# Kernel tuning notes

Measured on AMD Instinct MI355X. Metric: run time of the kernel, lower is better.

## Reference

```python
import jax, jax.numpy as jnp
import numpy as np

E = 1408      # hidden_size
H = 16        # num heads
D = E // H    # head_dim = 88
S = 1025      # (448/14)^2 + 1 cls token
B = 8


def setup_inputs() -> dict:
    key = jax.random.key(0)
    ks = jax.random.split(key, 11)
    scale = 1.0 / np.sqrt(E)
    inp = {
        "hidden_states": jax.random.normal(ks[0], (B, S, E), dtype=jnp.float32),
    }
    # rotary freqs as cos/sin of random angles, shape (S, D//2)
    theta = jax.random.uniform(ks[1], (S, D // 2), dtype=jnp.float32) * (2.0 * np.pi)
    inp["freqs_cos"] = jnp.cos(theta)
    inp["freqs_sin"] = jnp.sin(theta)
    # projection weights stored torch-style: (out_features, in_features)
    inp["q_w"] = jax.random.normal(ks[2], (E, E), dtype=jnp.float32) * scale
    inp["q_b"] = jax.random.normal(ks[3], (E,), dtype=jnp.float32) * scale
    inp["k_w"] = jax.random.normal(ks[4], (E, E), dtype=jnp.float32) * scale
    inp["k_b"] = jax.random.normal(ks[5], (E,), dtype=jnp.float32) * scale
    inp["v_w"] = jax.random.normal(ks[6], (E, E), dtype=jnp.float32) * scale
    inp["v_b"] = jax.random.normal(ks[7], (E,), dtype=jnp.float32) * scale
    inp["o_w"] = jax.random.normal(ks[8], (E, E), dtype=jnp.float32) * scale
    inp["o_b"] = jax.random.normal(ks[9], (E,), dtype=jnp.float32) * scale
    return inp


def _apply_rope(x, cos, sin):
    # x: (B, S, H, D); interpret last dim as D//2 complex pairs (re, im)
    xr = x.astype(jnp.float32).reshape(*x.shape[:-1], D // 2, 2)
    re, im = xr[..., 0], xr[..., 1]
    c = cos[None, :, None, :]  # broadcast over batch and heads
    s = sin[None, :, None, :]
    out_re = re * c - im * s
    out_im = re * s + im * c
    return jnp.stack([out_re, out_im], axis=-1).reshape(x.shape).astype(x.dtype)


def reference(hidden_states, freqs_cos, freqs_sin, q_w, q_b, k_w, k_b, v_w, v_b, o_w, o_b):
    b, s, _ = hidden_states.shape
    q = (hidden_states @ q_w.T + q_b).reshape(b, s, H, D)
    k = (hidden_states @ k_w.T + k_b).reshape(b, s, H, D)
    v = (hidden_states @ v_w.T + v_b).reshape(b, s, H, D)
    q = _apply_rope(q, freqs_cos, freqs_sin)
    k = _apply_rope(k, freqs_cos, freqs_sin)
    # (B, H, S, D)
    q = q.transpose(0, 2, 1, 3)
    k = k.transpose(0, 2, 1, 3)
    v = v.transpose(0, 2, 1, 3)
    scores = jnp.einsum('bhqd,bhkd->bhqk', q, k) / np.sqrt(D)
    attn = jax.nn.softmax(scores.astype(jnp.float32), axis=-1).astype(q.dtype)
    out = jnp.einsum('bhqk,bhkd->bqhd', attn, v).reshape(b, s, H * D)
    out = out @ o_w.T + o_b
    return out, attn
```

## Files before the change

kernel.cpp:

```cpp
#include <hip/hip_runtime.h>

typedef unsigned short u16;
typedef __attribute__((ext_vector_type(8))) short short8;
typedef __attribute__((ext_vector_type(4))) float f32x4;
typedef __attribute__((ext_vector_type(16))) float f32x16;

#define E_DIM 1408
#define H_HEADS 16
#define S_SEQ 1025
#define B_BATCH 8
#define S_PAD 1088
#define D_PAD 128
#define M_ROWS 8200
#define M_PAD 8320

struct __attribute__((packed, aligned(4))) f4u { float x, y, z, w; };

__device__ __forceinline__ u16 f2bf(float f){
  union { float f; unsigned u; } x; x.f = f;
  unsigned r = x.u + 0x7fffu + ((x.u >> 16) & 1u);
  return (u16)(r >> 16);
}

__device__ __forceinline__ void gload16(const void* g, void* l){
  __builtin_amdgcn_global_load_lds(
      (const __attribute__((address_space(1))) void*)g,
      (__attribute__((address_space(3))) void*)l, 16, 0, 0);
}

__device__ __forceinline__ f32x4 mfma16(short8 a, short8 b, f32x4 c){
  return __builtin_amdgcn_mfma_f32_16x16x32_bf16(a, b, c, 0, 0, 0);
}
__device__ __forceinline__ f32x16 mfma32(short8 a, short8 b, f32x16 c){
  return __builtin_amdgcn_mfma_f32_32x32x16_bf16(a, b, c, 0, 0, 0);
}

__device__ __forceinline__ unsigned cvtpk(float a, float b){
  unsigned r;
  asm("v_cvt_pk_bf16_f32 %0, %1, %2" : "=v"(r) : "v"(a), "v"(b));
  return r;
}
__device__ __forceinline__ void plswap(unsigned &a, unsigned &b){
  asm("v_permlane32_swap_b32 %0, %1" : "+v"(a), "+v"(b));
}

__global__ __launch_bounds__(256) void cvt_kernel(const float* __restrict__ src,
                                                  u16* __restrict__ dst, int n8){
  int i = blockIdx.x * 256 + threadIdx.x;
  if (i >= n8) return;
  const float4* s4 = (const float4*)src;
  float4 a = s4[2*i], b = s4[2*i+1];
  union { u16 u[8]; short8 v; } o;
  o.u[0]=f2bf(a.x); o.u[1]=f2bf(a.y); o.u[2]=f2bf(a.z); o.u[3]=f2bf(a.w);
  o.u[4]=f2bf(b.x); o.u[5]=f2bf(b.y); o.u[6]=f2bf(b.z); o.u[7]=f2bf(b.w);
  ((short8*)dst)[i] = o.v;
}

__global__ __launch_bounds__(256) void cvt4_kernel(const float* __restrict__ s0,
                                                   const float* __restrict__ s1,
                                                   const float* __restrict__ s2,
                                                   const float* __restrict__ s3,
                                                   u16* __restrict__ dst, int n8){
  int i = blockIdx.x * 256 + threadIdx.x;
  if (i >= n8) return;
  const float* src = (blockIdx.y == 0) ? s0 : (blockIdx.y == 1) ? s1
                   : (blockIdx.y == 2) ? s2 : s3;
  u16* d = dst + (size_t)blockIdx.y * n8 * 8;
  const float4* s4 = (const float4*)src;
  float4 a = s4[2*i], b = s4[2*i+1];
  union { u16 u[8]; short8 v; } o;
  o.u[0]=f2bf(a.x); o.u[1]=f2bf(a.y); o.u[2]=f2bf(a.z); o.u[3]=f2bf(a.w);
  o.u[4]=f2bf(b.x); o.u[5]=f2bf(b.y); o.u[6]=f2bf(b.z); o.u[7]=f2bf(b.w);
  ((short8*)d)[i] = o.v;
}

__global__ __launch_bounds__(256) void zero_pads_kernel(u16* __restrict__ Q,
                                                        u16* __restrict__ K,
                                                        u16* __restrict__ Vt){
  int i = blockIdx.x * 256 + threadIdx.x;
  const int n1 = 128 * S_PAD * 8;
  const int n2 = 128 * 63 * 96;
  const int n3 = 128 * 96 * 63;
  if (i < n1){
    int d = 88 + (i & 7); int t = i >> 3;
    int s = t % S_PAD; int bh = t / S_PAD;
    size_t o = ((size_t)bh * S_PAD + s) * D_PAD + d;
    Q[o] = 0; K[o] = 0;
  } else if (i < n1 + n2){
    int j = i - n1;
    int d = j % 96; int t = j / 96;
    int s = 1025 + t % 63; int bh = t / 63;
    size_t o = ((size_t)bh * S_PAD + s) * D_PAD + d;
    Q[o] = 0; K[o] = 0;
  } else if (i < n1 + n2 + n3){
    int j = i - n1 - n2;
    int d = j % 96; int t = j / 96;
    int sp = 1025 + t % 63; int bh = t / 63;
    Vt[((size_t)bh * D_PAD + d) * S_PAD + sp] = 0;
  }
}

template<int MODE>
__global__ __launch_bounds__(256) void gemm_bt(
    const u16* __restrict__ A, const u16* __restrict__ W,
    const float* __restrict__ b_q, const float* __restrict__ b_k,
    const float* __restrict__ b_v,
    u16* __restrict__ Qb, u16* __restrict__ Kb, u16* __restrict__ Vtb,
    float* __restrict__ outF,
    const float* __restrict__ fcos, const float* __restrict__ fsin)
{
  __shared__ u16 As[128*32];
  __shared__ u16 Bs[128*32];
  const int tid = threadIdx.x;
  const int lane = tid & 63, wid = tid >> 6;
  const int cl = lane & 15, grp = lane >> 4;

  const int nwg = (int)(gridDim.x * gridDim.y);
  const int orig = blockIdx.x + gridDim.x * blockIdx.y;
  const int qq = nwg >> 3, rr = nwg & 7;
  const int xcd = orig & 7, kk = orig >> 3;
  const int wg = (xcd < rr ? xcd * (qq + 1) : rr * (qq + 1) + (xcd - rr) * qq) + kk;
  const int bx = wg % (int)gridDim.x, by = wg / (int)gridDim.x;

  const int n0 = bx * 128, m0 = by * 128;
  const int region = (MODE == 0) ? (bx / 11) : 0;
  const int wm = (wid >> 1) * 64, wn = (wid & 1) * 64;
  f32x4 acc[4][4] = {};

  for (int k0 = 0; k0 < E_DIM; k0 += 32){
    __syncthreads();
#pragma unroll
    for (int rd = 0; rd < 2; ++rd){
      int G = rd * 256 + tid;
      int row = G >> 2, cg = G & 3;
      gload16(A + (size_t)(m0 + row) * E_DIM + k0 + cg * 8, (char*)As + (size_t)G * 16);
      gload16(W + (size_t)(n0 + row) * E_DIM + k0 + cg * 8, (char*)Bs + (size_t)G * 16);
    }
    __syncthreads();
    short8 av[4], bv[4];
#pragma unroll
    for (int i = 0; i < 4; ++i) av[i] = *(const short8*)&As[(wm + i*16 + cl)*32 + grp*8];
#pragma unroll
    for (int j = 0; j < 4; ++j) bv[j] = *(const short8*)&Bs[(wn + j*16 + cl)*32 + grp*8];
    __builtin_amdgcn_s_setprio(1);
#pragma unroll
    for (int i = 0; i < 4; ++i)
#pragma unroll
      for (int j = 0; j < 4; ++j)
        acc[i][j] = mfma16(av[i], bv[j], acc[i][j]);
    __builtin_amdgcn_s_setprio(0);
  }

  const float* bias = (MODE == 1) ? b_q : (region == 0 ? b_q : (region == 1 ? b_k : b_v));
  const float QSCALE = 0.15379181f;

#pragma unroll
  for (int i = 0; i < 4; ++i){
#pragma unroll
    for (int j = 0; j < 4; ++j){
      const int jcol = n0 + wn + j*16 + cl;
      const int jl = jcol - region * E_DIM;
      const float bsv = bias[jl];
      const int hh = jl / 88;
      const int dd = jl - hh * 88;
#pragma unroll
      for (int r = 0; r < 4; ++r){
        const int rrow = m0 + wm + i*16 + grp*4 + r;
        float v = acc[i][j][r] + bsv;
        if (MODE == 0 && region <= 1){
          float other = __shfl_xor(v, 1);
          int bb = rrow / 1025;
          int spos = rrow - bb * 1025;
          int pp = dd >> 1;
          float c = fcos[spos * 44 + pp];
          float s = fsin[spos * 44 + pp];
          float o = fmaf(v, c, (jl & 1) ? (other * s) : -(other * s));
          if (region == 0) o *= QSCALE;
          if (rrow < M_ROWS){
            size_t dst = (((size_t)(bb * 16 + hh)) * S_PAD + spos) * D_PAD + dd;
            (region ? Kb : Qb)[dst] = f2bf(o);
          }
        } else if (MODE == 0){
          if (rrow < M_ROWS){
            int bb = rrow / 1025;
            int spos = rrow - bb * 1025;
            size_t dst = (((size_t)(bb * 16 + hh)) * D_PAD + dd) * S_PAD + spos;
            Vtb[dst] = f2bf(v);
          }
        } else {
          if (rrow < M_ROWS) outF[(size_t)rrow * E_DIM + jcol] = v;
        }
      }
    }
  }
}

#define STAGE_K(buf, kt)                                                        \
  {                                                                             \
    _Pragma("unroll")                                                           \
    for (int rd = 0; rd < 4; ++rd){                                             \
      int G = rd * 256 + tid;                                                   \
      int row = G >> 4, c = G & 15;                                             \
      gload16(Kg + (size_t)((kt) * 64 + row) * 128 + ((c ^ (row & 15)) * 8),    \
              (char*)&Ks[buf][0] + (size_t)G * 16);                             \
    }                                                                           \
  }

#define STAGE_V(kt)                                                             \
  {                                                                             \
    _Pragma("unroll")                                                           \
    for (int rd = 0; rd < 3; ++rd){                                             \
      int G = rd * 256 + tid;                                                   \
      int row = G >> 3, c = G & 7;                                              \
      gload16(Vg + (size_t)row * S_PAD + (kt) * 64 + ((c ^ (row & 7)) * 8),     \
              (char*)Vs + (size_t)G * 16);                                      \
    }                                                                           \
  }

__global__ __launch_bounds__(256, 3) void attn_kernel(
    const u16* __restrict__ Qb, const u16* __restrict__ Kb,
    const u16* __restrict__ Vtb, float* __restrict__ attn,
    u16* __restrict__ AO)
{
  __shared__ u16 Ks[2][64 * 128];
  __shared__ u16 Vs[96 * 64];
  const int tid = threadIdx.x, wid = tid >> 6, lane = tid & 63;
  const int q5 = lane & 31, hi = lane >> 5;
  int lin = blockIdx.x + gridDim.x * blockIdx.y;
  lin = (lin & 7) * 144 + (lin >> 3);
  const int qt = lin % 9, bh = lin / 9;
  const int b = bh >> 4, h = bh & 15;
  const u16* __restrict__ Qg = Qb + (size_t)bh * S_PAD * 128;
  const u16* __restrict__ Kg = Kb + (size_t)bh * S_PAD * 128;
  const u16* __restrict__ Vg = Vtb + (size_t)bh * 128 * S_PAD;
  const int qrow = qt * 128 + wid * 32 + q5;
  const int qrowc = (qrow < S_PAD) ? qrow : (S_PAD - 1);

  short8 qf[6];
#pragma unroll
  for (int ds = 0; ds < 6; ++ds)
    qf[ds] = *(const short8*)&Qg[(size_t)qrowc * 128 + ds * 16 + hi * 8];

  float l0 = 0.f, l1 = 0.f, l2 = 0.f, l3 = 0.f;
  STAGE_K(0, 0);
  __syncthreads();
  for (int kt = 0; kt < 17; ++kt){
    const int cur = kt & 1;
    if (kt < 16) STAGE_K(cur ^ 1, kt + 1);
#pragma unroll
    for (int ks = 0; ks < 2; ++ks){
      f32x16 sc = {};
      const int krow = ks * 32 + q5;
      __builtin_amdgcn_s_setprio(1);
#pragma unroll
      for (int ds = 0; ds < 6; ++ds){
        int c = ds * 2 + hi;
        short8 kf = *(const short8*)&Ks[cur][krow * 128 + ((c ^ (krow & 15)) * 8)];
        sc = mfma32(kf, qf[ds], sc);
      }
      __builtin_amdgcn_s_setprio(0);
#pragma unroll
      for (int r = 0; r < 16; r += 4){
        l0 += __builtin_amdgcn_exp2f(sc[r]);
        l1 += __builtin_amdgcn_exp2f(sc[r+1]);
        l2 += __builtin_amdgcn_exp2f(sc[r+2]);
        l3 += __builtin_amdgcn_exp2f(sc[r+3]);
      }
    }
    __syncthreads();
  }
  float l = (l0 + l1) + (l2 + l3);
  l += __shfl_xor(l, 32);
  l -= 63.0f;
  const float lg2l = __builtin_amdgcn_logf(l);

  f32x16 oacc[3] = {};
  STAGE_K(0, 0);
  STAGE_V(0);
  __syncthreads();
  for (int kt = 0; kt < 17; ++kt){
    const int cur = kt & 1;
    if (kt < 16) STAGE_K(cur ^ 1, kt + 1);
    short8 pa0[2], pa1[2];
#pragma unroll
    for (int ks = 0; ks < 2; ++ks){
      f32x16 sc = {};
      const int krow = ks * 32 + q5;
      __builtin_amdgcn_s_setprio(1);
#pragma unroll
      for (int ds = 0; ds < 6; ++ds){
        int c = ds * 2 + hi;
        short8 kf = *(const short8*)&Ks[cur][krow * 128 + ((c ^ (krow & 15)) * 8)];
        sc = mfma32(kf, qf[ds], sc);
      }
      __builtin_amdgcn_s_setprio(0);
#pragma unroll
      for (int r = 0; r < 16; ++r) sc[r] = __builtin_amdgcn_exp2f(sc[r] - lg2l);

      if (qrow < 1025){
        if (kt < 16){
          float* arow = attn + ((size_t)bh * 1025 + qrow) * 1025 + kt * 64 + ks * 32 + 4 * hi;
#pragma unroll
          for (int g = 0; g < 4; ++g){
            f4u w4 = { sc[4*g], sc[4*g+1], sc[4*g+2], sc[4*g+3] };
            *(f4u*)(arow + 8 * g) = w4;
          }
        } else {
#pragma unroll
          for (int r = 0; r < 16; ++r){
            int kabs = 1024 + ks * 32 + (r & 3) + 8 * (r >> 2) + 4 * hi;
            if (kabs < 1025)
              attn[((size_t)bh * 1025 + qrow) * 1025 + kabs] = sc[r];
          }
        }
      }

      unsigned w0 = cvtpk(sc[0],  sc[1]),  w1 = cvtpk(sc[2],  sc[3]);
      unsigned w2 = cvtpk(sc[4],  sc[5]),  w3 = cvtpk(sc[6],  sc[7]);
      unsigned w4 = cvtpk(sc[8],  sc[9]),  w5 = cvtpk(sc[10], sc[11]);
      unsigned w6 = cvtpk(sc[12], sc[13]), w7 = cvtpk(sc[14], sc[15]);
      plswap(w0, w2); plswap(w1, w3); plswap(w4, w6); plswap(w5, w7);
      union U { unsigned u[4]; short8 s8; } A0, A1;
      A0.u[0] = w0; A0.u[1] = w1; A0.u[2] = w2; A0.u[3] = w3;
      A1.u[0] = w4; A1.u[1] = w5; A1.u[2] = w6; A1.u[3] = w7;
      pa0[ks] = A0.s8; pa1[ks] = A1.s8;
    }

    __syncthreads();
    __builtin_amdgcn_s_setprio(1);
#pragma unroll
    for (int ks = 0; ks < 2; ++ks){
#pragma unroll
      for (int dt = 0; dt < 3; ++dt){
        const int vrow = dt * 32 + q5;
        int c0 = ks * 4 + hi;
        short8 vf0 = *(const short8*)&Vs[vrow * 64 + ((c0 ^ (vrow & 7)) * 8)];
        oacc[dt] = mfma32(pa0[ks], vf0, oacc[dt]);
        int c1 = ks * 4 + 2 + hi;
        short8 vf1 = *(const short8*)&Vs[vrow * 64 + ((c1 ^ (vrow & 7)) * 8)];
        oacc[dt] = mfma32(pa1[ks], vf1, oacc[dt]);
      }
    }
    __builtin_amdgcn_s_setprio(0);
    __syncthreads();
    if (kt < 16) STAGE_V(kt + 1);
  }

  const int qb0 = qt * 128 + wid * 32;
#pragma unroll
  for (int dt = 0; dt < 3; ++dt){
    const int d = dt * 32 + q5;
    if (d < 88){
#pragma unroll
      for (int r = 0; r < 16; ++r){
        int qq2 = qb0 + (r & 3) + 8 * (r >> 2) + 4 * hi;
        if (qq2 < 1025)
          AO[((size_t)b * 1025 + qq2) * E_DIM + h * 88 + d] = f2bf(oacc[dt][r]);
      }
    }
  }
}

extern "C" void kernel_launch(void* const* d_in, const int* in_sizes, int n_in,
                              void* d_out, int out_size, void* d_ws, size_t ws_size,
                              hipStream_t stream)
{
  const float* hs   = (const float*)d_in[0];
  const float* fcos = (const float*)d_in[1];
  const float* fsin = (const float*)d_in[2];
  const float* q_w  = (const float*)d_in[3];
  const float* q_b  = (const float*)d_in[4];
  const float* k_w  = (const float*)d_in[5];
  const float* k_b  = (const float*)d_in[6];
  const float* v_w  = (const float*)d_in[7];
  const float* v_b  = (const float*)d_in[8];
  const float* o_w  = (const float*)d_in[9];
  const float* o_b  = (const float*)d_in[10];
  float* out0 = (float*)d_out;
  float* attn = out0 + (size_t)B_BATCH * S_SEQ * E_DIM;

  char* ws = (char*)d_ws;
  size_t off = 0;
  auto take = [&](size_t bytes){
    char* p = ws + off; off += (bytes + 255) & ~(size_t)255; return p;
  };
  u16* Xb  = (u16*)take((size_t)M_PAD * E_DIM * 2);
  u16* Wb  = (u16*)take((size_t)4 * E_DIM * E_DIM * 2);
  u16* Qb  = (u16*)take((size_t)128 * S_PAD * D_PAD * 2);
  u16* Kb  = (u16*)take((size_t)128 * S_PAD * D_PAD * 2);
  u16* Vtb = (u16*)take((size_t)128 * D_PAD * S_PAD * 2);
  u16* AO  = (u16*)take((size_t)M_PAD * E_DIM * 2);

  cvt_kernel<<<(1443200 + 255) / 256, 256, 0, stream>>>(hs, Xb, 1443200);
  cvt4_kernel<<<dim3(968, 4), 256, 0, stream>>>(q_w, k_w, v_w, o_w, Wb, 247808);
  zero_pads_kernel<<<10400, 256, 0, stream>>>(Qb, Kb, Vtb);

  gemm_bt<0><<<dim3(33, 65), 256, 0, stream>>>(Xb, Wb, q_b, k_b, v_b,
                                               Qb, Kb, Vtb, nullptr, fcos, fsin);

  attn_kernel<<<dim3(9, 128), 256, 0, stream>>>(Qb, Kb, Vtb, attn, AO);

  gemm_bt<1><<<dim3(11, 65), 256, 0, stream>>>(AO, Wb + 3 * (size_t)E_DIM * E_DIM,
                                               o_b, o_b, o_b,
                                               nullptr, nullptr, nullptr, out0, fcos, fsin);
}
```

Before: 547.9 us.

## Widen attention blocks to 512 threads with double-buffered K/V prefetch pipeline

Measured after the change: 561.3 us. 2.5% more time.

```diff
diff --git a/kernel.cpp b/kernel.cpp
--- a/kernel.cpp
+++ b/kernel.cpp
@@ -13,6 +13,7 @@
 #define D_PAD 128
 #define M_ROWS 8200
 #define M_PAD 8320
+#define N_QKV 4224
 
 struct __attribute__((packed, aligned(4))) f4u { float x, y, z, w; };
 
@@ -43,6 +44,9 @@
 __device__ __forceinline__ void plswap(unsigned &a, unsigned &b){
   asm("v_permlane32_swap_b32 %0, %1" : "+v"(a), "+v"(b));
 }
+
+#define BARX() { asm volatile("" ::: "memory"); __builtin_amdgcn_s_barrier(); asm volatile("" ::: "memory"); }
+#define WAITV(n) asm volatile("s_waitcnt vmcnt(" #n ")" ::: "memory")
 
 __global__ __launch_bounds__(256) void cvt_kernel(const float* __restrict__ src,
                                                   u16* __restrict__ dst, int n8){
@@ -56,15 +60,13 @@
   ((short8*)dst)[i] = o.v;
 }
 
-__global__ __launch_bounds__(256) void cvt4_kernel(const float* __restrict__ s0,
+__global__ __launch_bounds__(256) void cvt3_kernel(const float* __restrict__ s0,
                                                    const float* __restrict__ s1,
                                                    const float* __restrict__ s2,
-                                                   const float* __restrict__ s3,
                                                    u16* __restrict__ dst, int n8){
   int i = blockIdx.x * 256 + threadIdx.x;
   if (i >= n8) return;
-  const float* src = (blockIdx.y == 0) ? s0 : (blockIdx.y == 1) ? s1
-                   : (blockIdx.y == 2) ? s2 : s3;
+  const float* src = (blockIdx.y == 0) ? s0 : (blockIdx.y == 1) ? s1 : s2;
   u16* d = dst + (size_t)blockIdx.y * n8 * 8;
   const float4* s4 = (const float4*)src;
   float4 a = s4[2*i], b = s4[2*i+1];
@@ -198,42 +200,44 @@
 #define STAGE_K(buf, kt)                                                        \
   {                                                                             \
     _Pragma("unroll")                                                           \
-    for (int rd = 0; rd < 4; ++rd){                                             \
-      int G = rd * 256 + tid;                                                   \
+    for (int rd = 0; rd < 2; ++rd){                                             \
+      int G = rd * 512 + tid;                                                   \
       int row = G >> 4, c = G & 15;                                             \
       gload16(Kg + (size_t)((kt) * 64 + row) * 128 + ((c ^ (row & 15)) * 8),    \
-              (char*)&Ks[buf][0] + (size_t)G * 16);                             \
+              (char*)Ks + (size_t)(buf) * 16384 + (size_t)G * 16);              \
     }                                                                           \
   }
 
-#define STAGE_V(kt)                                                             \
+#define STAGE_V(buf, kt)                                                        \
   {                                                                             \
     _Pragma("unroll")                                                           \
-    for (int rd = 0; rd < 3; ++rd){                                             \
-      int G = rd * 256 + tid;                                                   \
+    for (int rd = 0; rd < 2; ++rd){                                             \
+      int G = rd * 512 + tid;                                                   \
       int row = G >> 3, c = G & 7;                                              \
       gload16(Vg + (size_t)row * S_PAD + (kt) * 64 + ((c ^ (row & 7)) * 8),     \
-              (char*)Vs + (size_t)G * 16);                                      \
+              (char*)Vs + (size_t)(buf) * 16384 + (size_t)G * 16);              \
     }                                                                           \
   }
 
-__global__ __launch_bounds__(256, 3) void attn_kernel(
+__global__ __launch_bounds__(512, 4) void attn_kernel(
     const u16* __restrict__ Qb, const u16* __restrict__ Kb,
     const u16* __restrict__ Vtb, float* __restrict__ attn,
     u16* __restrict__ AO)
 {
-  __shared__ u16 Ks[2][64 * 128];
-  __shared__ u16 Vs[96 * 64];
+  __shared__ u16 sm[32768];
+  u16* const Ks = sm;
+  u16* const Vs = sm + 16384;
   const int tid = threadIdx.x, wid = tid >> 6, lane = tid & 63;
   const int q5 = lane & 31, hi = lane >> 5;
   int lin = blockIdx.x + gridDim.x * blockIdx.y;
-  lin = (lin & 7) * 144 + (lin >> 3);
-  const int qt = lin % 9, bh = lin / 9;
+  lin = (lin & 7) * 80 + (lin >> 3);
+  const int qt = lin % 5, bh = lin / 5;
   const int b = bh >> 4, h = bh & 15;
   const u16* __restrict__ Qg = Qb + (size_t)bh * S_PAD * 128;
   const u16* __restrict__ Kg = Kb + (size_t)bh * S_PAD * 128;
   const u16* __restrict__ Vg = Vtb + (size_t)bh * 128 * S_PAD;
-  const int qrow = qt * 128 + wid * 32 + q5;
+  const int qb0 = qt * 256 + wid * 32;
+  const int qrow = qb0 + q5;
   const int qrowc = (qrow < S_PAD) ? qrow : (S_PAD - 1);
 
   short8 qf[6];
@@ -243,10 +247,11 @@
 
   float l0 = 0.f, l1 = 0.f, l2 = 0.f, l3 = 0.f;
   STAGE_K(0, 0);
-  __syncthreads();
+  STAGE_K(1, 1);
+  WAITV(2);
+  BARX();
   for (int kt = 0; kt < 17; ++kt){
     const int cur = kt & 1;
-    if (kt < 16) STAGE_K(cur ^ 1, kt + 1);
 #pragma unroll
     for (int ks = 0; ks < 2; ++ks){
       f32x16 sc = {};
@@ -255,7 +260,7 @@
 #pragma unroll
       for (int ds = 0; ds < 6; ++ds){
         int c = ds * 2 + hi;
-        short8 kf = *(const short8*)&Ks[cur][krow * 128 + ((c ^ (krow & 15)) * 8)];
+        short8 kf = *(const short8*)&Ks[(size_t)cur * 8192 + krow * 128 + ((c ^ (krow & 15)) * 8)];
         sc = mfma32(kf, qf[ds], sc);
       }
       __builtin_amdgcn_s_setprio(0);
@@ -267,20 +272,31 @@
         l3 += __builtin_amdgcn_exp2f(sc[r+3]);
       }
     }
-    __syncthreads();
-  }
+    if (kt == 16) break;
+    BARX();
+    if (kt <= 14){
+      STAGE_K(cur, kt + 2);
+      WAITV(2);
+    } else {
+      STAGE_V(0, 0);
+      STAGE_V(1, 1);
+      WAITV(4);
+    }
+    BARX();
+  }
+  BARX();
+  STAGE_K(0, 0);
+  STAGE_K(1, 1);
   float l = (l0 + l1) + (l2 + l3);
   l += __shfl_xor(l, 32);
   l -= 63.0f;
   const float lg2l = __builtin_amdgcn_logf(l);
+  WAITV(2);
+  BARX();
 
   f32x16 oacc[3] = {};
-  STAGE_K(0, 0);
-  STAGE_V(0);
-  __syncthreads();
   for (int kt = 0; kt < 17; ++kt){
     const int cur = kt & 1;
-    if (kt < 16) STAGE_K(cur ^ 1, kt + 1);
     short8 pa0[2], pa1[2];
 #pragma unroll
     for (int ks = 0; ks < 2; ++ks){
@@ -290,7 +306,7 @@
 #pragma unroll
       for (int ds = 0; ds < 6; ++ds){
         int c = ds * 2 + hi;
-        short8 kf = *(const short8*)&Ks[cur][krow * 128 + ((c ^ (krow & 15)) * 8)];
+        short8 kf = *(const short8*)&Ks[(size_t)cur * 8192 + krow * 128 + ((c ^ (krow & 15)) * 8)];
         sc = mfma32(kf, qf[ds], sc);
       }
       __builtin_amdgcn_s_setprio(0);
@@ -326,7 +342,6 @@
       pa0[ks] = A0.s8; pa1[ks] = A1.s8;
     }
 
-    __syncthreads();
     __builtin_amdgcn_s_setprio(1);
 #pragma unroll
     for (int ks = 0; ks < 2; ++ks){
@@ -334,19 +349,27 @@
       for (int dt = 0; dt < 3; ++dt){
         const int vrow = dt * 32 + q5;
         int c0 = ks * 4 + hi;
-        short8 vf0 = *(const short8*)&Vs[vrow * 64 + ((c0 ^ (vrow & 7)) * 8)];
+        short8 vf0 = *(const short8*)&Vs[(size_t)cur * 8192 + vrow * 64 + ((c0 ^ (vrow & 7)) * 8)];
         oacc[dt] = mfma32(pa0[ks], vf0, oacc[dt]);
         int c1 = ks * 4 + 2 + hi;
-        short8 vf1 = *(const short8*)&Vs[vrow * 64 + ((c1 ^ (vrow & 7)) * 8)];
+        short8 vf1 = *(const short8*)&Vs[(size_t)cur * 8192 + vrow * 64 + ((c1 ^ (vrow & 7)) * 8)];
         oacc[dt] = mfma32(pa1[ks], vf1, oacc[dt]);
       }
     }
     __builtin_amdgcn_s_setprio(0);
-    __syncthreads();
-    if (kt < 16) STAGE_V(kt + 1);
-  }
-
-  const int qb0 = qt * 128 + wid * 32;
+
+    if (kt == 16) break;
+    BARX();
+    if (kt <= 14){
+      STAGE_K(cur, kt + 2);
+      STAGE_V(cur, kt + 2);
+      WAITV(4);
+    } else {
+      WAITV(0);
+    }
+    BARX();
+  }
+
 #pragma unroll
   for (int dt = 0; dt < 3; ++dt){
     const int d = dt * 32 + q5;
@@ -384,23 +407,24 @@
   auto take = [&](size_t bytes){
     char* p = ws + off; off += (bytes + 255) & ~(size_t)255; return p;
   };
-  u16* Xb  = (u16*)take((size_t)M_PAD * E_DIM * 2);
-  u16* Wb  = (u16*)take((size_t)4 * E_DIM * E_DIM * 2);
-  u16* Qb  = (u16*)take((size_t)128 * S_PAD * D_PAD * 2);
-  u16* Kb  = (u16*)take((size_t)128 * S_PAD * D_PAD * 2);
-  u16* Vtb = (u16*)take((size_t)128 * D_PAD * S_PAD * 2);
-  u16* AO  = (u16*)take((size_t)M_PAD * E_DIM * 2);
+  u16* Xb   = (u16*)take((size_t)M_PAD * E_DIM * 2);
+  u16* Wqkv = (u16*)take((size_t)N_QKV * E_DIM * 2);
+  u16* Wo   = (u16*)take((size_t)E_DIM * E_DIM * 2);
+  u16* Qb   = (u16*)take((size_t)128 * S_PAD * D_PAD * 2);
+  u16* Kb   = (u16*)take((size_t)128 * S_PAD * D_PAD * 2);
+  u16* Vtb  = (u16*)take((size_t)128 * D_PAD * S_PAD * 2);
+  u16* AO   = (u16*)take((size_t)M_PAD * E_DIM * 2);
 
   cvt_kernel<<<(1443200 + 255) / 256, 256, 0, stream>>>(hs, Xb, 1443200);
-  cvt4_kernel<<<dim3(968, 4), 256, 0, stream>>>(q_w, k_w, v_w, o_w, Wb, 247808);
+  cvt3_kernel<<<dim3(968, 3), 256, 0, stream>>>(q_w, k_w, v_w, Wqkv, 247808);
+  cvt_kernel<<<968, 256, 0, stream>>>(o_w, Wo, 247808);
   zero_pads_kernel<<<10400, 256, 0, stream>>>(Qb, Kb, Vtb);
 
-  gemm_bt<0><<<dim3(33, 65), 256, 0, stream>>>(Xb, Wb, q_b, k_b, v_b,
+  gemm_bt<0><<<dim3(33, 65), 256, 0, stream>>>(Xb, Wqkv, q_b, k_b, v_b,
                                                Qb, Kb, Vtb, nullptr, fcos, fsin);
 
-  attn_kernel<<<dim3(9, 128), 256, 0, stream>>>(Qb, Kb, Vtb, attn, AO);
-
-  gemm_bt<1><<<dim3(11, 65), 256, 0, stream>>>(AO, Wb + 3 * (size_t)E_DIM * E_DIM,
-                                               o_b, o_b, o_b,
+  attn_kernel<<<dim3(5, 128), 512, 0, stream>>>(Qb, Kb, Vtb, attn, AO);
+
+  gemm_bt<1><<<dim3(11, 65), 256, 0, stream>>>(AO, Wo, o_b, o_b, o_b,
                                                nullptr, nullptr, nullptr, out0, fcos, fsin);
 }
```

## Split V projection into transposed GEMM and pipeline attention loads with vmcnt waits

Applied to the files above, without the earlier changes.

Result: no change. 557.2 us (+1.7%).

```diff
diff --git a/kernel.cpp b/kernel.cpp
--- a/kernel.cpp
+++ b/kernel.cpp
@@ -13,6 +13,7 @@
 #define D_PAD 128
 #define M_ROWS 8200
 #define M_PAD 8320
+#define N_QKV 4224
 
 struct __attribute__((packed, aligned(4))) f4u { float x, y, z, w; };
 
@@ -43,6 +44,9 @@
 __device__ __forceinline__ void plswap(unsigned &a, unsigned &b){
   asm("v_permlane32_swap_b32 %0, %1" : "+v"(a), "+v"(b));
 }
+
+#define BARX() { asm volatile("" ::: "memory"); __builtin_amdgcn_s_barrier(); asm volatile("" ::: "memory"); }
+#define WAITV(n) asm volatile("s_waitcnt vmcnt(" #n ")" ::: "memory")
 
 __global__ __launch_bounds__(256) void cvt_kernel(const float* __restrict__ src,
                                                   u16* __restrict__ dst, int n8){
@@ -56,15 +60,13 @@
   ((short8*)dst)[i] = o.v;
 }
 
-__global__ __launch_bounds__(256) void cvt4_kernel(const float* __restrict__ s0,
+__global__ __launch_bounds__(256) void cvt3_kernel(const float* __restrict__ s0,
                                                    const float* __restrict__ s1,
                                                    const float* __restrict__ s2,
-                                                   const float* __restrict__ s3,
                                                    u16* __restrict__ dst, int n8){
   int i = blockIdx.x * 256 + threadIdx.x;
   if (i >= n8) return;
-  const float* src = (blockIdx.y == 0) ? s0 : (blockIdx.y == 1) ? s1
-                   : (blockIdx.y == 2) ? s2 : s3;
+  const float* src = (blockIdx.y == 0) ? s0 : (blockIdx.y == 1) ? s1 : s2;
   u16* d = dst + (size_t)blockIdx.y * n8 * 8;
   const float4* s4 = (const float4*)src;
   float4 a = s4[2*i], b = s4[2*i+1];
@@ -151,8 +153,32 @@
     __builtin_amdgcn_s_setprio(0);
   }
 
-  const float* bias = (MODE == 1) ? b_q : (region == 0 ? b_q : (region == 1 ? b_k : b_v));
   const float QSCALE = 0.15379181f;
+
+  if (MODE == 2){
+#pragma unroll
+    for (int j = 0; j < 4; ++j){
+      const int scol = n0 + wn + j*16 + cl;
+      const int bb = scol / 1025;
+      const int spos = scol - bb * 1025;
+      const bool ok = (scol < M_ROWS);
+#pragma unroll
+      for (int i = 0; i < 4; ++i){
+#pragma unroll
+        for (int r = 0; r < 4; ++r){
+          const int jl = m0 + wm + i*16 + grp*4 + r;
+          const int hh = jl / 88;
+          const int dd = jl - hh * 88;
+          float v = acc[i][j][r] + b_v[jl];
+          if (ok)
+            Vtb[(((size_t)(bb * 16 + hh)) * D_PAD + dd) * S_PAD + spos] = f2bf(v);
+        }
+      }
+    }
+    return;
+  }
+
+  const float* bias = (MODE == 1) ? b_q : (region == 0 ? b_q : b_k);
 
 #pragma unroll
   for (int i = 0; i < 4; ++i){
@@ -167,7 +193,7 @@
       for (int r = 0; r < 4; ++r){
         const int rrow = m0 + wm + i*16 + grp*4 + r;
         float v = acc[i][j][r] + bsv;
-        if (MODE == 0 && region <= 1){
+        if (MODE == 0){
           float other = __shfl_xor(v, 1);
           int bb = rrow / 1025;
           int spos = rrow - bb * 1025;
@@ -180,13 +206,6 @@
             size_t dst = (((size_t)(bb * 16 + hh)) * S_PAD + spos) * D_PAD + dd;
             (region ? Kb : Qb)[dst] = f2bf(o);
           }
-        } else if (MODE == 0){
-          if (rrow < M_ROWS){
-            int bb = rrow / 1025;
-            int spos = rrow - bb * 1025;
-            size_t dst = (((size_t)(bb * 16 + hh)) * D_PAD + dd) * S_PAD + spos;
-            Vtb[dst] = f2bf(v);
-          }
         } else {
           if (rrow < M_ROWS) outF[(size_t)rrow * E_DIM + jcol] = v;
         }
@@ -220,7 +239,7 @@
 __global__ __launch_bounds__(256, 3) void attn_kernel(
     const u16* __restrict__ Qb, const u16* __restrict__ Kb,
     const u16* __restrict__ Vtb, float* __restrict__ attn,
-    u16* __restrict__ AO)
+    u16* __restrict__ AO, float* __restrict__ dumpf)
 {
   __shared__ u16 Ks[2][64 * 128];
   __shared__ u16 Vs[96 * 64];
@@ -233,7 +252,8 @@
   const u16* __restrict__ Qg = Qb + (size_t)bh * S_PAD * 128;
   const u16* __restrict__ Kg = Kb + (size_t)bh * S_PAD * 128;
   const u16* __restrict__ Vg = Vtb + (size_t)bh * 128 * S_PAD;
-  const int qrow = qt * 128 + wid * 32 + q5;
+  const int qb0 = qt * 128 + wid * 32;
+  const int qrow = qb0 + q5;
   const int qrowc = (qrow < S_PAD) ? qrow : (S_PAD - 1);
 
   short8 qf[6];
@@ -243,10 +263,15 @@
 
   float l0 = 0.f, l1 = 0.f, l2 = 0.f, l3 = 0.f;
   STAGE_K(0, 0);
-  __syncthreads();
   for (int kt = 0; kt < 17; ++kt){
     const int cur = kt & 1;
-    if (kt < 16) STAGE_K(cur ^ 1, kt + 1);
+    if (kt < 16){
+      STAGE_K(cur ^ 1, kt + 1);
+      WAITV(4);
+    } else {
+      WAITV(0);
+    }
+    BARX();
 #pragma unroll
     for (int ks = 0; ks < 2; ++ks){
       f32x16 sc = {};
@@ -267,7 +292,7 @@
         l3 += __builtin_amdgcn_exp2f(sc[r+3]);
       }
     }
-    __syncthreads();
+    BARX();
   }
   float l = (l0 + l1) + (l2 + l3);
   l += __shfl_xor(l, 32);
@@ -277,10 +302,13 @@
   f32x16 oacc[3] = {};
   STAGE_K(0, 0);
   STAGE_V(0);
-  __syncthreads();
   for (int kt = 0; kt < 17; ++kt){
     const int cur = kt & 1;
     if (kt < 16) STAGE_K(cur ^ 1, kt + 1);
+    if (kt == 0)      { WAITV(7); }
+    else if (kt < 16) { WAITV(15); }
+    else              { WAITV(11); }
+    BARX();
     short8 pa0[2], pa1[2];
 #pragma unroll
     for (int ks = 0; ks < 2; ++ks){
@@ -297,21 +325,23 @@
 #pragma unroll
       for (int r = 0; r < 16; ++r) sc[r] = __builtin_amdgcn_exp2f(sc[r] - lg2l);
 
-      if (qrow < 1025){
-        if (kt < 16){
-          float* arow = attn + ((size_t)bh * 1025 + qrow) * 1025 + kt * 64 + ks * 32 + 4 * hi;
-#pragma unroll
-          for (int g = 0; g < 4; ++g){
-            f4u w4 = { sc[4*g], sc[4*g+1], sc[4*g+2], sc[4*g+3] };
-            *(f4u*)(arow + 8 * g) = w4;
-          }
-        } else {
-#pragma unroll
-          for (int r = 0; r < 16; ++r){
-            int kabs = 1024 + ks * 32 + (r & 3) + 8 * (r >> 2) + 4 * hi;
-            if (kabs < 1025)
-              attn[((size_t)bh * 1025 + qrow) * 1025 + kabs] = sc[r];
-          }
+      if (kt < 16){
+        float* arow = (qrow < 1025)
+          ? attn + ((size_t)bh * 1025 + qrow) * 1025 + kt * 64 + ks * 32 + 4 * hi
+          : dumpf + tid * 16;
+#pragma unroll
+        for (int g = 0; g < 4; ++g){
+          f4u w4 = { sc[4*g], sc[4*g+1], sc[4*g+2], sc[4*g+3] };
+          *(f4u*)(arow + 8 * g) = w4;
+        }
+      } else {
+#pragma unroll
+        for (int r = 0; r < 16; ++r){
+          int kabs = 1024 + ks * 32 + (r & 3) + 8 * (r >> 2) + 4 * hi;
+          float* ad = (qrow < 1025 && kabs < 1025)
+            ? attn + ((size_t)bh * 1025 + qrow) * 1025 + kabs
+            : dumpf + tid;
+          *ad = sc[r];
         }
       }
 
@@ -326,7 +356,8 @@
       pa0[ks] = A0.s8; pa1[ks] = A1.s8;
     }
 
-    __syncthreads();
+    if (kt < 16) { WAITV(12); } else { WAITV(0); }
+    BARX();
     __builtin_amdgcn_s_setprio(1);
 #pragma unroll
     for (int ks = 0; ks < 2; ++ks){
@@ -342,11 +373,10 @@
       }
     }
     __builtin_amdgcn_s_setprio(0);
-    __syncthreads();
+    BARX();
     if (kt < 16) STAGE_V(kt + 1);
   }
 
-  const int qb0 = qt * 128 + wid * 32;
 #pragma unroll
   for (int dt = 0; dt < 3; ++dt){
     const int d = dt * 32 + q5;
@@ -384,23 +414,28 @@
   auto take = [&](size_t bytes){
     char* p = ws + off; off += (bytes + 255) & ~(size_t)255; return p;
   };
-  u16* Xb  = (u16*)take((size_t)M_PAD * E_DIM * 2);
-  u16* Wb  = (u16*)take((size_t)4 * E_DIM * E_DIM * 2);
-  u16* Qb  = (u16*)take((size_t)128 * S_PAD * D_PAD * 2);
-  u16* Kb  = (u16*)take((size_t)128 * S_PAD * D_PAD * 2);
-  u16* Vtb = (u16*)take((size_t)128 * D_PAD * S_PAD * 2);
-  u16* AO  = (u16*)take((size_t)M_PAD * E_DIM * 2);
+  u16* Xb   = (u16*)take((size_t)M_PAD * E_DIM * 2);
+  u16* Wqkv = (u16*)take((size_t)N_QKV * E_DIM * 2);
+  u16* Wo   = (u16*)take((size_t)E_DIM * E_DIM * 2);
+  u16* Qb   = (u16*)take((size_t)128 * S_PAD * D_PAD * 2);
+  u16* Kb   = (u16*)take((size_t)128 * S_PAD * D_PAD * 2);
+  u16* Vtb  = (u16*)take((size_t)128 * D_PAD * S_PAD * 2);
+  u16* AO   = (u16*)take((size_t)M_PAD * E_DIM * 2);
+  float* dumpf = (float*)take(65536);
 
   cvt_kernel<<<(1443200 + 255) / 256, 256, 0, stream>>>(hs, Xb, 1443200);
-  cvt4_kernel<<<dim3(968, 4), 256, 0, stream>>>(q_w, k_w, v_w, o_w, Wb, 247808);
+  cvt3_kernel<<<dim3(968, 3), 256, 0, stream>>>(q_w, k_w, v_w, Wqkv, 247808);
+  cvt_kernel<<<968, 256, 0, stream>>>(o_w, Wo, 247808);
   zero_pads_kernel<<<10400, 256, 0, stream>>>(Qb, Kb, Vtb);
 
-  gemm_bt<0><<<dim3(33, 65), 256, 0, stream>>>(Xb, Wb, q_b, k_b, v_b,
+  gemm_bt<0><<<dim3(22, 65), 256, 0, stream>>>(Xb, Wqkv, q_b, k_b, v_b,
                                                Qb, Kb, Vtb, nullptr, fcos, fsin);
-
-  attn_kernel<<<dim3(9, 128), 256, 0, stream>>>(Qb, Kb, Vtb, attn, AO);
-
-  gemm_bt<1><<<dim3(11, 65), 256, 0, stream>>>(AO, Wb + 3 * (size_t)E_DIM * E_DIM,
-                                               o_b, o_b, o_b,
+  gemm_bt<2><<<dim3(65, 11), 256, 0, stream>>>(Wqkv + 2 * (size_t)E_DIM * E_DIM, Xb,
+                                               q_b, k_b, v_b,
+                                               Qb, Kb, Vtb, nullptr, fcos, fsin);
+
+  attn_kernel<<<dim3(9, 128), 256, 0, stream>>>(Qb, Kb, Vtb, attn, AO, dumpf);
+
+  gemm_bt<1><<<dim3(11, 65), 256, 0, stream>>>(AO, Wo, o_b, o_b, o_b,
                                                nullptr, nullptr, nullptr, out0, fcos, fsin);
 }
```
